# Performance work log

Measured on AMD Instinct MI355X. Metric: run time of the kernel, lower is better.

The kernel has to match this reference:

```python
import jax, jax.numpy as jnp
import numpy as np

B, T, D, H = 2, 2048, 768, 12
HS = D // H


def setup_inputs() -> dict:
    key = jax.random.key(0)
    ks = jax.random.split(key, 11)
    s = 1.0 / np.sqrt(D)
    return {
        "query": jax.random.normal(ks[0], (B, T, D), jnp.float32),
        "key": jax.random.normal(ks[1], (B, T, D), jnp.float32),
        "value": jax.random.normal(ks[2], (B, T, D), jnp.float32),
        "Wq": jax.random.normal(ks[3], (D, D), jnp.float32) * s,
        "bq": jax.random.normal(ks[4], (D,), jnp.float32) * s,
        "Wk": jax.random.normal(ks[5], (D, D), jnp.float32) * s,
        "bk": jax.random.normal(ks[6], (D,), jnp.float32) * s,
        "Wv": jax.random.normal(ks[7], (D, D), jnp.float32) * s,
        "bv": jax.random.normal(ks[8], (D,), jnp.float32) * s,
        "Wo": jax.random.normal(ks[9], (D, D), jnp.float32) * s,
        "bo": jax.random.normal(ks[10], (D,), jnp.float32) * s,
    }


def reference(query, key, value, Wq, bq, Wk, bk, Wv, bv, Wo, bo):
    # Projections (torch nn.Linear: x @ W.T + b), then split heads -> [B,H,T,HS]
    def split_heads(x):
        return x.reshape(B, -1, H, HS).transpose(0, 2, 1, 3)

    q = split_heads(query @ Wq.T + bq)
    k = split_heads(key @ Wk.T + bk)
    v = split_heads(value @ Wv.T + bv)

    scale = 1.0 / jnp.sqrt(jnp.asarray(HS, q.dtype))
    scores = jnp.einsum("bhqd,bhkd->bhqk", q, k) * scale  # [B,H,Tq,Tk]
    attn = jax.nn.softmax(scores, axis=-1)
    out = jnp.einsum("bhqk,bhkd->bhqd", attn, v)  # [B,H,Tq,HS]
    out = out.transpose(0, 2, 1, 3).reshape(B, -1, D)
    output = out @ Wo.T + bo
    return output, attn.mean(axis=1)
```

## Files before the change

### kernel.cpp

```cpp
#include <hip/hip_runtime.h>
#include <hip/hip_fp16.h>
#include <stdint.h>

typedef _Float16 f16;
typedef _Float16 f16x8 __attribute__((ext_vector_type(8)));
typedef _Float16 f16x4v __attribute__((ext_vector_type(4)));
typedef __fp16 h16x2 __attribute__((ext_vector_type(2)));
typedef float f32x4 __attribute__((ext_vector_type(4)));
typedef float f32x16 __attribute__((ext_vector_type(16)));

#define MFMA16(a,b,c) __builtin_amdgcn_mfma_f32_16x16x32_f16(a,b,c,0,0,0)
#define MFMA32(a,b,c) __builtin_amdgcn_mfma_f32_32x32x16_f16(a,b,c,0,0,0)
#define CVTPK(a,b) __builtin_amdgcn_cvt_pkrtz(a,b)

#if __has_builtin(__builtin_amdgcn_exp2f)
#define EXP2(x) __builtin_amdgcn_exp2f(x)
#else
#define EXP2(x) exp2f(x)
#endif

static __device__ __forceinline__ float dot2acc(h16x2 a, float c) {
#if __has_builtin(__builtin_amdgcn_fdot2)
    const h16x2 one = { (__fp16)1.f, (__fp16)1.f };
    return __builtin_amdgcn_fdot2(a, one, c, false);
#else
    return c + (float)a[0] + (float)a[1];
#endif
}

typedef __attribute__((address_space(1))) void gvoid_t;
typedef __attribute__((address_space(3))) void svoid_t;
#define AS1(p) ((gvoid_t*)(uintptr_t)(p))
#define AS3(p) ((svoid_t*)(uint32_t)(uintptr_t)(p))

static constexpr int Bc = 2, Tc = 2048, Dc = 768, Hc = 12;
static constexpr int Mc = Bc * Tc;
static constexpr float SC2 = 0.18033688011112042f;

union PA { f16x8 v; h16x2 h[4]; };

#define FRAG32(BASE, ROWOFF, CHUNK) \
    (*(const f16x8*)((const char*)(BASE) + \
        ((ROWOFF) + q32) * 128 + (((CHUNK) ^ g7) * 16)))

__global__ __launch_bounds__(256) void conv_all(
    const float* __restrict__ q, const float* __restrict__ k, const float* __restrict__ v,
    const float* __restrict__ wq, const float* __restrict__ wk, const float* __restrict__ wv,
    const float* __restrict__ wo,
    f16* __restrict__ qh, f16* __restrict__ kh, f16* __restrict__ vh,
    f16* __restrict__ wqh, f16* __restrict__ wkh, f16* __restrict__ wvh, f16* __restrict__ woh)
{
    const int NI = (Mc * Dc) / 4;
    const int NW = (Dc * Dc) / 4;
    int i = blockIdx.x * 256 + threadIdx.x;
    if (i >= 3 * NI + 4 * NW) return;
    const float4* src; f16* dst; int j; float scl = 1.f;
    if (i < 3 * NI) {
        int a = i / NI; j = i - a * NI;
        src = (const float4*)(a == 0 ? q : (a == 1 ? k : v));
        dst = (a == 0 ? qh : (a == 1 ? kh : vh));
    } else {
        int t = i - 3 * NI;
        int a = t / NW; j = t - a * NW;
        src = (const float4*)(a == 0 ? wq : (a == 1 ? wk : (a == 2 ? wv : wo)));
        dst = (a == 0 ? wqh : (a == 1 ? wkh : (a == 2 ? wvh : woh)));
        if (a == 0) scl = SC2;
    }
    float4 f = src[j];
    f16x4v o = { (f16)(f.x * scl), (f16)(f.y * scl), (f16)(f.z * scl), (f16)(f.w * scl) };
    *(f16x4v*)(dst + 4 * j) = o;
}

__device__ __forceinline__ void gemm_tile_mainloop(
    const f16* __restrict__ A, const f16* __restrict__ W,
    int brow, int bcol, f16* As, f16* Bs, f32x4 acc[4][4])
{
    const int tid = threadIdx.x;
    const int w = tid >> 6, lane = tid & 63;
    const int lg = lane & 15, hg = lane >> 4;
    const int wr = w >> 1, wc = w & 1;

    for (int kt = 0; kt < 768 / 32; ++kt) {
        const int k0 = kt * 32;
#pragma unroll
        for (int j = 0; j < 2; ++j) {
            int p = (w * 2 + j) * 1024 + lane * 16;
            int r = p >> 6;
            int ke = (p & 63) >> 1;
            __builtin_amdgcn_global_load_lds(AS1(A + (size_t)(brow + r) * 768 + k0 + ke),
                                             AS3((char*)As + (w * 2 + j) * 1024), 16, 0, 0);
            __builtin_amdgcn_global_load_lds(AS1(W + (size_t)(bcol + r) * 768 + k0 + ke),
                                             AS3((char*)Bs + (w * 2 + j) * 1024), 16, 0, 0);
        }
        __syncthreads();
        f16x8 af[4], bf[4];
#pragma unroll
        for (int m = 0; m < 4; ++m)
            af[m] = *(const f16x8*)(As + (wr * 64 + m * 16 + lg) * 32 + hg * 8);
#pragma unroll
        for (int n = 0; n < 4; ++n)
            bf[n] = *(const f16x8*)(Bs + (wc * 64 + n * 16 + lg) * 32 + hg * 8);
#pragma unroll
        for (int m = 0; m < 4; ++m)
#pragma unroll
            for (int n = 0; n < 4; ++n)
                acc[m][n] = MFMA16(af[m], bf[n], acc[m][n]);
        __syncthreads();
    }
}

__global__ __launch_bounds__(256) void qkv_proj(
    const f16* __restrict__ qh, const f16* __restrict__ kh, const f16* __restrict__ vh,
    const f16* __restrict__ wqh, const f16* __restrict__ wkh, const f16* __restrict__ wvh,
    const float* __restrict__ bq, const float* __restrict__ bk, const float* __restrict__ bv,
    f16* __restrict__ Qp, f16* __restrict__ Kp, f16* __restrict__ Vt)
{
    __shared__ f16 As[128 * 32], Bs[128 * 32];
    const int z = blockIdx.z;
    const f16* A = (z == 0) ? qh : (z == 1) ? kh : vh;
    const f16* W = (z == 0) ? wqh : (z == 1) ? wkh : wvh;
    const float* bias = (z == 0) ? bq : (z == 1) ? bk : bv;
    const int brow = blockIdx.y * 128, bcol = blockIdx.x * 128;

    f32x4 acc[4][4];
    const f32x4 z4 = { 0.f, 0.f, 0.f, 0.f };
#pragma unroll
    for (int m = 0; m < 4; ++m)
#pragma unroll
        for (int n = 0; n < 4; ++n) acc[m][n] = z4;

    gemm_tile_mainloop(A, W, brow, bcol, As, Bs, acc);

    const int tid = threadIdx.x, w = tid >> 6, lane = tid & 63;
    const int lg = lane & 15, hg = lane >> 4, wr = w >> 1, wc = w & 1;
#pragma unroll
    for (int n = 0; n < 4; ++n) {
        const int c = bcol + wc * 64 + n * 16 + lg;
        const float bval = (z == 0) ? bias[c] * SC2 : bias[c];
#pragma unroll
        for (int m = 0; m < 4; ++m) {
            const int r0 = brow + wr * 64 + m * 16 + hg * 4;
#pragma unroll
            for (int r = 0; r < 4; ++r) {
                const float val = acc[m][n][r] + bval;
                const int row = r0 + r;
                if (z == 0) {
                    Qp[(size_t)row * 768 + c] = (f16)val;
                } else if (z == 1) {
                    Kp[(size_t)row * 768 + c] = (f16)val;
                } else {
                    const int bb = row >> 11, t = row & 2047;
                    const int hh = c >> 6, d = c & 63;
                    const int tl = t & 31;
                    const int sw = ((tl >> 2) ^ (tl >> 3)) & 1;
                    const int tp = (t & ~31) | (tl ^ (sw * 12));
                    Vt[(((size_t)(bb * 12 + hh)) * 64 + d) * 2048 + tp] = (f16)val;
                }
            }
        }
    }
}

__global__ __launch_bounds__(256) void out_proj(
    const f16* __restrict__ ctx, const f16* __restrict__ woh,
    const float* __restrict__ bo, float* __restrict__ out)
{
    __shared__ f16 As[128 * 32], Bs[128 * 32];
    const int brow = blockIdx.y * 128, bcol = blockIdx.x * 128;
    f32x4 acc[4][4];
    const f32x4 z4 = { 0.f, 0.f, 0.f, 0.f };
#pragma unroll
    for (int m = 0; m < 4; ++m)
#pragma unroll
        for (int n = 0; n < 4; ++n) acc[m][n] = z4;

    gemm_tile_mainloop(ctx, woh, brow, bcol, As, Bs, acc);

    const int tid = threadIdx.x, w = tid >> 6, lane = tid & 63;
    const int lg = lane & 15, hg = lane >> 4, wr = w >> 1, wc = w & 1;
#pragma unroll
    for (int n = 0; n < 4; ++n) {
        const int c = bcol + wc * 64 + n * 16 + lg;
        const float bval = bo[c];
#pragma unroll
        for (int m = 0; m < 4; ++m) {
            const int r0 = brow + wr * 64 + m * 16 + hg * 4;
#pragma unroll
            for (int r = 0; r < 4; ++r)
                out[(size_t)(r0 + r) * 768 + c] = acc[m][n][r] + bval;
        }
    }
}

__global__ __launch_bounds__(256, 3) void attn_out(
    const f16* __restrict__ Qp, const f16* __restrict__ Kp, const f16* __restrict__ Vt,
    float* __restrict__ l_inv, f16* __restrict__ ctx)
{
    __shared__ f16 Kbuf[2][4096];
    __shared__ f16 Vbuf[2][4096];
    __shared__ float Ored[2][32][64];
    __shared__ float lred[2][2][32];

    const int qt = blockIdx.x, h = blockIdx.y, b = blockIdx.z;
    const int tid = threadIdx.x, w = tid >> 6, lane = tid & 63;
    const int q32 = lane & 31, hi = lane >> 5, g7 = lane & 7;
    const int qh = w & 1, kh = w >> 1;
    const int wbase16 = (tid & ~63) * 16;

    const size_t qrow0 = (size_t)b * 2048 + qt * 64 + qh * 32;
    const int hcol = h * 64;

    const f16* qb = Qp + (qrow0 + q32) * 768 + hcol + hi * 8;
    f16x8 bqf[4];
#pragma unroll
    for (int d = 0; d < 4; ++d) bqf[d] = *(const f16x8*)(qb + d * 16);

    const size_t kbase = (size_t)b * 2048;
    const f16* Vg = Vt + ((size_t)(b * 12 + h)) * 64 * 2048;

    f32x16 oacc[2];
#pragma unroll
    for (int dt = 0; dt < 2; ++dt)
#pragma unroll
        for (int r = 0; r < 16; ++r) oacc[dt][r] = 0.f;
    float lsum = 0.f;

#define STAGE_KV(KT_, BUF) do { \
    _Pragma("unroll") \
    for (int j_ = 0; j_ < 2; ++j_) { \
        const int p_ = j_ * 256 + tid; \
        const int row_ = p_ >> 3, c_ = (p_ & 7) ^ (row_ & 7); \
        __builtin_amdgcn_global_load_lds( \
            AS1(Kp + (kbase + (size_t)(KT_) * 64 + row_) * 768 + hcol + c_ * 8), \
            AS3((char*)&Kbuf[BUF][0] + j_ * 4096 + wbase16), 16, 0, 0); \
        __builtin_amdgcn_global_load_lds( \
            AS1(Vg + (size_t)row_ * 2048 + (KT_) * 64 + c_ * 8), \
            AS3((char*)&Vbuf[BUF][0] + j_ * 4096 + wbase16), 16, 0, 0); \
    } } while (0)

#define AOBODY(CUR) do { \
    const f16* Kb_ = &Kbuf[CUR][0]; const f16* Vb_ = &Vbuf[CUR][0]; \
    f32x16 sa; \
    _Pragma("unroll") \
    for (int r_ = 0; r_ < 16; ++r_) sa[r_] = 0.f; \
    sa = MFMA32(FRAG32(Kb_, kh * 32, 0 + hi), bqf[0], sa); \
    sa = MFMA32(FRAG32(Kb_, kh * 32, 2 + hi), bqf[1], sa); \
    sa = MFMA32(FRAG32(Kb_, kh * 32, 4 + hi), bqf[2], sa); \
    sa = MFMA32(FRAG32(Kb_, kh * 32, 6 + hi), bqf[3], sa); \
    float p[16]; \
    _Pragma("unroll") \
    for (int r_ = 0; r_ < 16; ++r_) p[r_] = EXP2(sa[r_]); \
    PA pa0, pa1; \
    pa0.h[0] = CVTPK(p[0], p[1]);   pa0.h[1] = CVTPK(p[2], p[3]); \
    pa0.h[2] = CVTPK(p[4], p[5]);   pa0.h[3] = CVTPK(p[6], p[7]); \
    pa1.h[0] = CVTPK(p[8], p[9]);   pa1.h[1] = CVTPK(p[10], p[11]); \
    pa1.h[2] = CVTPK(p[12], p[13]); pa1.h[3] = CVTPK(p[14], p[15]); \
    float t0_ = 0.f, t1_ = 0.f; \
    t0_ = dot2acc(pa0.h[0], t0_); t0_ = dot2acc(pa0.h[1], t0_); \
    t0_ = dot2acc(pa0.h[2], t0_); t0_ = dot2acc(pa0.h[3], t0_); \
    t1_ = dot2acc(pa1.h[0], t1_); t1_ = dot2acc(pa1.h[1], t1_); \
    t1_ = dot2acc(pa1.h[2], t1_); t1_ = dot2acc(pa1.h[3], t1_); \
    lsum += t0_ + t1_; \
    oacc[0] = MFMA32(FRAG32(Vb_, 0,  kh * 4 + 0 + hi), pa0.v, oacc[0]); \
    oacc[0] = MFMA32(FRAG32(Vb_, 0,  kh * 4 + 2 + hi), pa1.v, oacc[0]); \
    oacc[1] = MFMA32(FRAG32(Vb_, 32, kh * 4 + 0 + hi), pa0.v, oacc[1]); \
    oacc[1] = MFMA32(FRAG32(Vb_, 32, kh * 4 + 2 + hi), pa1.v, oacc[1]); \
} while (0)

    STAGE_KV(0, 0);
    __syncthreads();
    for (int kt = 0; kt < 32; ++kt) {
        const int cur = kt & 1;
        if (kt < 31) STAGE_KV(kt + 1, cur ^ 1);
        AOBODY(cur);
        __syncthreads();
    }
#undef STAGE_KV
#undef AOBODY

    lsum += __shfl_xor(lsum, 32);
    if (hi == 0) lred[kh][qh][q32] = lsum;
    if (kh == 1) {
#pragma unroll
        for (int dt = 0; dt < 2; ++dt)
#pragma unroll
            for (int g = 0; g < 4; ++g) {
                float4 v4 = { oacc[dt][g * 4 + 0], oacc[dt][g * 4 + 1],
                              oacc[dt][g * 4 + 2], oacc[dt][g * 4 + 3] };
                *(float4*)&Ored[qh][q32][dt * 32 + g * 8 + hi * 4] = v4;
            }
    }
    __syncthreads();
    if (kh == 0) {
        const float iv = 1.f / (lred[0][qh][q32] + lred[1][qh][q32]);
        if (hi == 0)
            l_inv[((size_t)(b * 12 + h)) * 2048 + qt * 64 + qh * 32 + q32] = iv;
        f16* cb = ctx + (qrow0 + q32) * 768 + hcol;
#pragma unroll
        for (int dt = 0; dt < 2; ++dt)
#pragma unroll
            for (int g = 0; g < 4; ++g) {
                const int d0 = dt * 32 + g * 8 + hi * 4;
                const float4 o4 = *(const float4*)&Ored[qh][q32][d0];
                f16x4v s;
#pragma unroll
                for (int e = 0; e < 4; ++e)
                    s[e] = (f16)((oacc[dt][g * 4 + e] + (&o4.x)[e]) * iv);
                *(f16x4v*)(cb + d0) = s;
            }
    }
}

__global__ __launch_bounds__(128, 2) void attn_mean(
    const f16* __restrict__ Qp, const f16* __restrict__ Kp,
    const float* __restrict__ l_inv, float* __restrict__ om)
{
    __shared__ f16 Qbuf[2][4096];
    __shared__ f16 Kbuf[2][4096];

    const int kt = blockIdx.x, qt = blockIdx.y, b = blockIdx.z;
    const int tid = threadIdx.x, lane = tid & 63;
    const int q32 = lane & 31, hi = lane >> 5, g7 = lane & 7;
    const int qh = tid >> 6;
    const int wb = (tid & 64) * 16;

    const size_t qtrow = (size_t)b * 2048 + qt * 64;
    const size_t ktrow = (size_t)b * 2048 + kt * 64;

    f32x16 macc[2];
#pragma unroll
    for (int kk = 0; kk < 2; ++kk)
#pragma unroll
        for (int r = 0; r < 16; ++r) macc[kk][r] = 0.f;

#define STAGE_QK(H_, BUF) do { \
    _Pragma("unroll") \
    for (int j_ = 0; j_ < 4; ++j_) { \
        const int p_ = j_ * 128 + tid; \
        const int row_ = p_ >> 3, c_ = (p_ & 7) ^ (row_ & 7); \
        __builtin_amdgcn_global_load_lds( \
            AS1(Qp + (qtrow + row_) * 768 + (H_) * 64 + c_ * 8), \
            AS3((char*)&Qbuf[BUF][0] + j_ * 2048 + wb), 16, 0, 0); \
        __builtin_amdgcn_global_load_lds( \
            AS1(Kp + (ktrow + row_) * 768 + (H_) * 64 + c_ * 8), \
            AS3((char*)&Kbuf[BUF][0] + j_ * 2048 + wb), 16, 0, 0); \
    } } while (0)

#define MBODY(H_, CUR) do { \
    const f16* Qb_ = &Qbuf[CUR][0]; const f16* Kb_ = &Kbuf[CUR][0]; \
    f16x8 qf[4]; \
    _Pragma("unroll") \
    for (int d_ = 0; d_ < 4; ++d_) qf[d_] = FRAG32(Qb_, qh * 32, d_ * 2 + hi); \
    f32x16 sa0, sa1; \
    _Pragma("unroll") \
    for (int r_ = 0; r_ < 16; ++r_) { sa0[r_] = 0.f; sa1[r_] = 0.f; } \
    sa0 = MFMA32(FRAG32(Kb_, 0,  0 + hi), qf[0], sa0); \
    sa0 = MFMA32(FRAG32(Kb_, 0,  2 + hi), qf[1], sa0); \
    sa0 = MFMA32(FRAG32(Kb_, 0,  4 + hi), qf[2], sa0); \
    sa0 = MFMA32(FRAG32(Kb_, 0,  6 + hi), qf[3], sa0); \
    sa1 = MFMA32(FRAG32(Kb_, 32, 0 + hi), qf[0], sa1); \
    sa1 = MFMA32(FRAG32(Kb_, 32, 2 + hi), qf[1], sa1); \
    sa1 = MFMA32(FRAG32(Kb_, 32, 4 + hi), qf[2], sa1); \
    sa1 = MFMA32(FRAG32(Kb_, 32, 6 + hi), qf[3], sa1); \
    const float ivv = l_inv[((size_t)(b * 12 + (H_))) * 2048 + qt * 64 + qh * 32 + q32]; \
    _Pragma("unroll") \
    for (int r_ = 0; r_ < 16; ++r_) { \
        macc[0][r_] += EXP2(sa0[r_]) * ivv; \
        macc[1][r_] += EXP2(sa1[r_]) * ivv; } \
} while (0)

    STAGE_QK(0, 0);
    __syncthreads();
    for (int h = 0; h < 12; ++h) {
        const int cur = h & 1;
        if (h < 11) STAGE_QK(h + 1, cur ^ 1);
        MBODY(h, cur);
        __syncthreads();
    }
#undef STAGE_QK
#undef MBODY

    float* ob = om + ((size_t)(b * 2048 + qt * 64 + qh * 32 + q32)) * 2048 + kt * 64;
#pragma unroll
    for (int kk = 0; kk < 2; ++kk)
#pragma unroll
        for (int g = 0; g < 4; ++g) {
            float4 v4 = { macc[kk][g * 4 + 0] * (1.0f / 12.0f),
                          macc[kk][g * 4 + 1] * (1.0f / 12.0f),
                          macc[kk][g * 4 + 2] * (1.0f / 12.0f),
                          macc[kk][g * 4 + 3] * (1.0f / 12.0f) };
            *(float4*)(ob + kk * 32 + g * 8 + hi * 4) = v4;
        }
}

extern "C" void kernel_launch(void* const* d_in, const int* in_sizes, int n_in,
                              void* d_out, int out_size, void* d_ws, size_t ws_size,
                              hipStream_t stream) {
    const float* q  = (const float*)d_in[0];
    const float* k  = (const float*)d_in[1];
    const float* v  = (const float*)d_in[2];
    const float* Wq = (const float*)d_in[3];
    const float* bq = (const float*)d_in[4];
    const float* Wk = (const float*)d_in[5];
    const float* bk = (const float*)d_in[6];
    const float* Wv = (const float*)d_in[7];
    const float* bv = (const float*)d_in[8];
    const float* Wo = (const float*)d_in[9];
    const float* bo = (const float*)d_in[10];
    float* out = (float*)d_out;

    char* ws = (char*)d_ws;
    const size_t SZ_IN = (size_t)Mc * Dc * 2;
    const size_t SZ_W  = (size_t)Dc * Dc * 2;
    f16* qh  = (f16*)(ws);
    f16* kh  = (f16*)(ws + SZ_IN);
    f16* vh  = (f16*)(ws + 2 * SZ_IN);
    f16* wqh = (f16*)(ws + 3 * SZ_IN);
    f16* wkh = (f16*)(ws + 3 * SZ_IN + SZ_W);
    f16* wvh = (f16*)(ws + 3 * SZ_IN + 2 * SZ_W);
    f16* woh = (f16*)(ws + 3 * SZ_IN + 3 * SZ_W);
    f16* Qp  = (f16*)(ws + 3 * SZ_IN + 4 * SZ_W);
    f16* Kp  = (f16*)(ws + 4 * SZ_IN + 4 * SZ_W);
    f16* Vt  = (f16*)(ws + 5 * SZ_IN + 4 * SZ_W);
    f16* ctx = qh;
    float* l_inv = (float*)kh;

    conv_all<<<dim3(11520), dim3(256), 0, stream>>>(q, k, v, Wq, Wk, Wv, Wo,
                                                    qh, kh, vh, wqh, wkh, wvh, woh);
    qkv_proj<<<dim3(6, 32, 3), dim3(256), 0, stream>>>(qh, kh, vh, wqh, wkh, wvh,
                                                       bq, bk, bv, Qp, Kp, Vt);
    attn_out<<<dim3(32, 12, 2), dim3(256), 0, stream>>>(Qp, Kp, Vt, l_inv, ctx);
    attn_mean<<<dim3(32, 32, 2), dim3(128), 0, stream>>>(Qp, Kp, l_inv,
                                                         out + (size_t)Mc * Dc);
    out_proj<<<dim3(6, 32, 1), dim3(256), 0, stream>>>(ctx, woh, bo, out);
}
```

Before: 145.2 us.

## Double-buffer GEMM mainloop and fuse out_proj with attn_mean into one launch

The shared GEMM mainloop now double-buffers its LDS tiles, so the next k-slice loads while the current one is multiplied. out_proj and attn_mean are merged into a single tail kernel: the first 192 blocks do the output projection and the rest compute the head-averaged attention probabilities. The attention-mean part changes from 128-thread blocks covering a 64x64 tile to 256-thread blocks in which each wave computes a 32x32 quadrant. The aim is to overlap the two independent tail workloads, drop a launch, and hide global-to-LDS latency in the GEMMs. The cost is doubled LDS use per GEMM block, which may reduce occupancy.

```diff
diff --git a/kernel.cpp b/kernel.cpp
--- a/kernel.cpp
+++ b/kernel.cpp
@@ -71,7 +71,7 @@
     *(f16x4v*)(dst + 4 * j) = o;
 }
 
-__device__ __forceinline__ void gemm_tile_mainloop(
+__device__ __forceinline__ void gemm_tile_mainloop_db(
     const f16* __restrict__ A, const f16* __restrict__ W,
     int brow, int bcol, f16* As, f16* Bs, f32x4 acc[4][4])
 {
@@ -80,26 +80,33 @@
     const int lg = lane & 15, hg = lane >> 4;
     const int wr = w >> 1, wc = w & 1;
 
-    for (int kt = 0; kt < 768 / 32; ++kt) {
-        const int k0 = kt * 32;
-#pragma unroll
-        for (int j = 0; j < 2; ++j) {
-            int p = (w * 2 + j) * 1024 + lane * 16;
-            int r = p >> 6;
-            int ke = (p & 63) >> 1;
-            __builtin_amdgcn_global_load_lds(AS1(A + (size_t)(brow + r) * 768 + k0 + ke),
-                                             AS3((char*)As + (w * 2 + j) * 1024), 16, 0, 0);
-            __builtin_amdgcn_global_load_lds(AS1(W + (size_t)(bcol + r) * 768 + k0 + ke),
-                                             AS3((char*)Bs + (w * 2 + j) * 1024), 16, 0, 0);
-        }
-        __syncthreads();
+#define GS(KT_, BUF_) do { \
+    const int k0_ = (KT_) * 32; \
+    _Pragma("unroll") \
+    for (int j_ = 0; j_ < 2; ++j_) { \
+        int p_ = (w * 2 + j_) * 1024 + lane * 16; \
+        int r_ = p_ >> 6; \
+        int ke_ = (p_ & 63) >> 1; \
+        __builtin_amdgcn_global_load_lds(AS1(A + (size_t)(brow + r_) * 768 + k0_ + ke_), \
+            AS3((char*)As + (BUF_) * 8192 + (w * 2 + j_) * 1024), 16, 0, 0); \
+        __builtin_amdgcn_global_load_lds(AS1(W + (size_t)(bcol + r_) * 768 + k0_ + ke_), \
+            AS3((char*)Bs + (BUF_) * 8192 + (w * 2 + j_) * 1024), 16, 0, 0); \
+    } } while (0)
+
+    GS(0, 0);
+    __syncthreads();
+    for (int kt = 0; kt < 24; ++kt) {
+        const int cur = kt & 1;
+        if (kt < 23) GS(kt + 1, cur ^ 1);
+        const f16* As_ = As + cur * 4096;
+        const f16* Bs_ = Bs + cur * 4096;
         f16x8 af[4], bf[4];
 #pragma unroll
         for (int m = 0; m < 4; ++m)
-            af[m] = *(const f16x8*)(As + (wr * 64 + m * 16 + lg) * 32 + hg * 8);
+            af[m] = *(const f16x8*)(As_ + (wr * 64 + m * 16 + lg) * 32 + hg * 8);
 #pragma unroll
         for (int n = 0; n < 4; ++n)
-            bf[n] = *(const f16x8*)(Bs + (wc * 64 + n * 16 + lg) * 32 + hg * 8);
+            bf[n] = *(const f16x8*)(Bs_ + (wc * 64 + n * 16 + lg) * 32 + hg * 8);
 #pragma unroll
         for (int m = 0; m < 4; ++m)
 #pragma unroll
@@ -107,6 +114,7 @@
                 acc[m][n] = MFMA16(af[m], bf[n], acc[m][n]);
         __syncthreads();
     }
+#undef GS
 }
 
 __global__ __launch_bounds__(256) void qkv_proj(
@@ -115,7 +123,7 @@
     const float* __restrict__ bq, const float* __restrict__ bk, const float* __restrict__ bv,
     f16* __restrict__ Qp, f16* __restrict__ Kp, f16* __restrict__ Vt)
 {
-    __shared__ f16 As[128 * 32], Bs[128 * 32];
+    __shared__ f16 As[2][4096], Bs[2][4096];
     const int z = blockIdx.z;
     const f16* A = (z == 0) ? qh : (z == 1) ? kh : vh;
     const f16* W = (z == 0) ? wqh : (z == 1) ? wkh : wvh;
@@ -129,7 +137,7 @@
 #pragma unroll
         for (int n = 0; n < 4; ++n) acc[m][n] = z4;
 
-    gemm_tile_mainloop(A, W, brow, bcol, As, Bs, acc);
+    gemm_tile_mainloop_db(A, W, brow, bcol, &As[0][0], &Bs[0][0], acc);
 
     const int tid = threadIdx.x, w = tid >> 6, lane = tid & 63;
     const int lg = lane & 15, hg = lane >> 4, wr = w >> 1, wc = w & 1;
@@ -161,37 +169,6 @@
     }
 }
 
-__global__ __launch_bounds__(256) void out_proj(
-    const f16* __restrict__ ctx, const f16* __restrict__ woh,
-    const float* __restrict__ bo, float* __restrict__ out)
-{
-    __shared__ f16 As[128 * 32], Bs[128 * 32];
-    const int brow = blockIdx.y * 128, bcol = blockIdx.x * 128;
-    f32x4 acc[4][4];
-    const f32x4 z4 = { 0.f, 0.f, 0.f, 0.f };
-#pragma unroll
-    for (int m = 0; m < 4; ++m)
-#pragma unroll
-        for (int n = 0; n < 4; ++n) acc[m][n] = z4;
-
-    gemm_tile_mainloop(ctx, woh, brow, bcol, As, Bs, acc);
-
-    const int tid = threadIdx.x, w = tid >> 6, lane = tid & 63;
-    const int lg = lane & 15, hg = lane >> 4, wr = w >> 1, wc = w & 1;
-#pragma unroll
-    for (int n = 0; n < 4; ++n) {
-        const int c = bcol + wc * 64 + n * 16 + lg;
-        const float bval = bo[c];
-#pragma unroll
-        for (int m = 0; m < 4; ++m) {
-            const int r0 = brow + wr * 64 + m * 16 + hg * 4;
-#pragma unroll
-            for (int r = 0; r < 4; ++r)
-                out[(size_t)(r0 + r) * 768 + c] = acc[m][n][r] + bval;
-        }
-    }
-}
-
 __global__ __launch_bounds__(256, 3) void attn_out(
     const f16* __restrict__ Qp, const f16* __restrict__ Kp, const f16* __restrict__ Vt,
     float* __restrict__ l_inv, f16* __restrict__ ctx)
@@ -311,86 +288,108 @@
     }
 }
 
-__global__ __launch_bounds__(128, 2) void attn_mean(
+__global__ __launch_bounds__(256) void tail_fused(
+    const f16* __restrict__ ctx, const f16* __restrict__ woh,
+    const float* __restrict__ bo, float* __restrict__ out,
     const f16* __restrict__ Qp, const f16* __restrict__ Kp,
     const float* __restrict__ l_inv, float* __restrict__ om)
 {
-    __shared__ f16 Qbuf[2][4096];
-    __shared__ f16 Kbuf[2][4096];
-
-    const int kt = blockIdx.x, qt = blockIdx.y, b = blockIdx.z;
-    const int tid = threadIdx.x, lane = tid & 63;
-    const int q32 = lane & 31, hi = lane >> 5, g7 = lane & 7;
-    const int qh = tid >> 6;
-    const int wb = (tid & 64) * 16;
-
-    const size_t qtrow = (size_t)b * 2048 + qt * 64;
-    const size_t ktrow = (size_t)b * 2048 + kt * 64;
-
-    f32x16 macc[2];
-#pragma unroll
-    for (int kk = 0; kk < 2; ++kk)
-#pragma unroll
-        for (int r = 0; r < 16; ++r) macc[kk][r] = 0.f;
-
-#define STAGE_QK(H_, BUF) do { \
-    _Pragma("unroll") \
-    for (int j_ = 0; j_ < 4; ++j_) { \
-        const int p_ = j_ * 128 + tid; \
+    __shared__ f16 sh[4][4096];
+
+    const int tid = threadIdx.x, w = tid >> 6, lane = tid & 63;
+
+    if (blockIdx.x < 192) {
+        const int brow = (blockIdx.x / 6) * 128, bcol = (blockIdx.x % 6) * 128;
+        f32x4 acc[4][4];
+        const f32x4 z4 = { 0.f, 0.f, 0.f, 0.f };
+#pragma unroll
+        for (int m = 0; m < 4; ++m)
+#pragma unroll
+            for (int n = 0; n < 4; ++n) acc[m][n] = z4;
+
+        gemm_tile_mainloop_db(ctx, woh, brow, bcol, &sh[0][0], &sh[2][0], acc);
+
+        const int lg = lane & 15, hg = lane >> 4, wr = w >> 1, wc = w & 1;
+#pragma unroll
+        for (int n = 0; n < 4; ++n) {
+            const int c = bcol + wc * 64 + n * 16 + lg;
+            const float bval = bo[c];
+#pragma unroll
+            for (int m = 0; m < 4; ++m) {
+                const int r0 = brow + wr * 64 + m * 16 + hg * 4;
+#pragma unroll
+                for (int r = 0; r < 4; ++r)
+                    out[(size_t)(r0 + r) * 768 + c] = acc[m][n][r] + bval;
+            }
+        }
+    } else {
+        const int mb = blockIdx.x - 192;
+        const int kt = mb & 31, r2 = mb >> 5;
+        const int qt = r2 & 31, b = r2 >> 5;
+        const int q32 = lane & 31, hi = lane >> 5, g7 = lane & 7;
+        const int qh = w & 1, kh = w >> 1;
+        const int wbase16 = (tid & ~63) * 16;
+
+        const size_t qtrow = (size_t)b * 2048 + qt * 64;
+        const size_t ktrow = (size_t)b * 2048 + kt * 64;
+
+        f32x16 macc;
+#pragma unroll
+        for (int r = 0; r < 16; ++r) macc[r] = 0.f;
+
+#define MSTAGE(H_, BUF) do { \
+    _Pragma("unroll") \
+    for (int j_ = 0; j_ < 2; ++j_) { \
+        const int p_ = j_ * 256 + tid; \
         const int row_ = p_ >> 3, c_ = (p_ & 7) ^ (row_ & 7); \
         __builtin_amdgcn_global_load_lds( \
             AS1(Qp + (qtrow + row_) * 768 + (H_) * 64 + c_ * 8), \
-            AS3((char*)&Qbuf[BUF][0] + j_ * 2048 + wb), 16, 0, 0); \
+            AS3((char*)&sh[0][0] + (BUF) * 8192 + j_ * 4096 + wbase16), 16, 0, 0); \
         __builtin_amdgcn_global_load_lds( \
             AS1(Kp + (ktrow + row_) * 768 + (H_) * 64 + c_ * 8), \
-            AS3((char*)&Kbuf[BUF][0] + j_ * 2048 + wb), 16, 0, 0); \
+            AS3((char*)&sh[2][0] + (BUF) * 8192 + j_ * 4096 + wbase16), 16, 0, 0); \
     } } while (0)
 
 #define MBODY(H_, CUR) do { \
-    const f16* Qb_ = &Qbuf[CUR][0]; const f16* Kb_ = &Kbuf[CUR][0]; \
+    const f16* Qb_ = (const f16*)((const char*)&sh[0][0] + (CUR) * 8192); \
+    const f16* Kb_ = (const f16*)((const char*)&sh[2][0] + (CUR) * 8192); \
     f16x8 qf[4]; \
     _Pragma("unroll") \
     for (int d_ = 0; d_ < 4; ++d_) qf[d_] = FRAG32(Qb_, qh * 32, d_ * 2 + hi); \
-    f32x16 sa0, sa1; \
-    _Pragma("unroll") \
-    for (int r_ = 0; r_ < 16; ++r_) { sa0[r_] = 0.f; sa1[r_] = 0.f; } \
-    sa0 = MFMA32(FRAG32(Kb_, 0,  0 + hi), qf[0], sa0); \
-    sa0 = MFMA32(FRAG32(Kb_, 0,  2 + hi), qf[1], sa0); \
-    sa0 = MFMA32(FRAG32(Kb_, 0,  4 + hi), qf[2], sa0); \
-    sa0 = MFMA32(FRAG32(Kb_, 0,  6 + hi), qf[3], sa0); \
-    sa1 = MFMA32(FRAG32(Kb_, 32, 0 + hi), qf[0], sa1); \
-    sa1 = MFMA32(FRAG32(Kb_, 32, 2 + hi), qf[1], sa1); \
-    sa1 = MFMA32(FRAG32(Kb_, 32, 4 + hi), qf[2], sa1); \
-    sa1 = MFMA32(FRAG32(Kb_, 32, 6 + hi), qf[3], sa1); \
+    f32x16 sa; \
+    _Pragma("unroll") \
+    for (int r_ = 0; r_ < 16; ++r_) sa[r_] = 0.f; \
+    sa = MFMA32(FRAG32(Kb_, kh * 32, 0 + hi), qf[0], sa); \
+    sa = MFMA32(FRAG32(Kb_, kh * 32, 2 + hi), qf[1], sa); \
+    sa = MFMA32(FRAG32(Kb_, kh * 32, 4 + hi), qf[2], sa); \
+    sa = MFMA32(FRAG32(Kb_, kh * 32, 6 + hi), qf[3], sa); \
     const float ivv = l_inv[((size_t)(b * 12 + (H_))) * 2048 + qt * 64 + qh * 32 + q32]; \
     _Pragma("unroll") \
-    for (int r_ = 0; r_ < 16; ++r_) { \
-        macc[0][r_] += EXP2(sa0[r_]) * ivv; \
-        macc[1][r_] += EXP2(sa1[r_]) * ivv; } \
+    for (int r_ = 0; r_ < 16; ++r_) macc[r_] += EXP2(sa[r_]) * ivv; \
 } while (0)
 
-    STAGE_QK(0, 0);
-    __syncthreads();
-    for (int h = 0; h < 12; ++h) {
-        const int cur = h & 1;
-        if (h < 11) STAGE_QK(h + 1, cur ^ 1);
-        MBODY(h, cur);
+        MSTAGE(0, 0);
         __syncthreads();
-    }
-#undef STAGE_QK
+        for (int h = 0; h < 12; ++h) {
+            const int cur = h & 1;
+            if (h < 11) MSTAGE(h + 1, cur ^ 1);
+            MBODY(h, cur);
+            __syncthreads();
+        }
+#undef MSTAGE
 #undef MBODY
 
-    float* ob = om + ((size_t)(b * 2048 + qt * 64 + qh * 32 + q32)) * 2048 + kt * 64;
-#pragma unroll
-    for (int kk = 0; kk < 2; ++kk)
+        float* ob = om + ((size_t)(b * 2048 + qt * 64 + qh * 32 + q32)) * 2048
+                  + kt * 64 + kh * 32;
 #pragma unroll
         for (int g = 0; g < 4; ++g) {
-            float4 v4 = { macc[kk][g * 4 + 0] * (1.0f / 12.0f),
-                          macc[kk][g * 4 + 1] * (1.0f / 12.0f),
-                          macc[kk][g * 4 + 2] * (1.0f / 12.0f),
-                          macc[kk][g * 4 + 3] * (1.0f / 12.0f) };
-            *(float4*)(ob + kk * 32 + g * 8 + hi * 4) = v4;
+            float4 v4 = { macc[g * 4 + 0] * (1.0f / 12.0f),
+                          macc[g * 4 + 1] * (1.0f / 12.0f),
+                          macc[g * 4 + 2] * (1.0f / 12.0f),
+                          macc[g * 4 + 3] * (1.0f / 12.0f) };
+            *(float4*)(ob + g * 8 + hi * 4) = v4;
         }
+    }
 }
 
 extern "C" void kernel_launch(void* const* d_in, const int* in_sizes, int n_in,
@@ -430,7 +429,7 @@
     qkv_proj<<<dim3(6, 32, 3), dim3(256), 0, stream>>>(qh, kh, vh, wqh, wkh, wvh,
                                                        bq, bk, bv, Qp, Kp, Vt);
     attn_out<<<dim3(32, 12, 2), dim3(256), 0, stream>>>(Qp, Kp, Vt, l_inv, ctx);
-    attn_mean<<<dim3(32, 32, 2), dim3(128), 0, stream>>>(Qp, Kp, l_inv,
-                                                         out + (size_t)Mc * Dc);
-    out_proj<<<dim3(6, 32, 1), dim3(256), 0, stream>>>(ctx, woh, bo, out);
-}
+    tail_fused<<<dim3(2240), dim3(256), 0, stream>>>(ctx, woh, bo, out,
+                                                     Qp, Kp, l_inv,
+                                                     out + (size_t)Mc * Dc);
+}
```

Result: faster. 131.2 us (-9.7%).
